# Optimization experiments

Hardware: AMD Instinct MI355X
Metric: run time of the kernel (lower is better)

## Reference

```python
import jax, jax.numpy as jnp
import numpy as np

IN_F = 4096
OUT_F = 4096
N = 16384


def setup_inputs() -> dict:
    key = jax.random.key(0)
    ks = jax.random.split(key, 7)
    return {
        "x": jax.random.normal(ks[0], (N, IN_F), dtype=jnp.float32),
        "weight_mu": jax.random.normal(ks[1], (OUT_F, IN_F), dtype=jnp.float32) * 0.1,
        "weight_rho": jax.random.normal(ks[2], (OUT_F, IN_F), dtype=jnp.float32) * 0.1,
        "bias_mu": jax.random.normal(ks[3], (OUT_F,), dtype=jnp.float32) * 0.1,
        "bias_rho": jax.random.normal(ks[4], (OUT_F,), dtype=jnp.float32) * 0.1,
        "eps_w": jax.random.normal(ks[5], (OUT_F, IN_F), dtype=jnp.float32),
        "eps_b": jax.random.normal(ks[6], (OUT_F,), dtype=jnp.float32),
    }


def reference(x, weight_mu, weight_rho, bias_mu, bias_rho, eps_w, eps_b):
    # softplus: log(1 + exp(rho)), written as log1p(exp(.)) for stability
    weight = weight_mu + jnp.log1p(jnp.exp(weight_rho)) * eps_w  # [out, in]
    bias = bias_mu + jnp.log1p(jnp.exp(bias_rho)) * eps_b        # [out]
    # F.linear(x, W, b) = x @ W.T + b
    return jnp.einsum("ni,oi->no", x, weight) + bias
```

## Files before the change

kernel.cpp:

```cpp
#include <hip/hip_runtime.h>
#include <hip/hip_bf16.h>

typedef unsigned short u16;
typedef __attribute__((ext_vector_type(4))) float f32x4;
typedef __attribute__((ext_vector_type(8))) short bf16x8;

__device__ __forceinline__ u16 f2bf(float f) {
    union { float f; unsigned u; } v; v.f = f;
    unsigned r = (v.u + 0x7fffu + ((v.u >> 16) & 1u)) >> 16;
    return (u16)r;
}

__device__ __forceinline__ float softplus(float x) {
    return (x > 15.f) ? x : log1pf(__expf(x));
}

__device__ __forceinline__ void gload_lds16(const void* g, void* l) {
    __builtin_amdgcn_global_load_lds(
        (__attribute__((address_space(1))) void*)(g),
        (__attribute__((address_space(3))) void*)(l),
        16, 0, 0);
}

#define BAR() do { asm volatile("" ::: "memory"); \
                   __builtin_amdgcn_s_barrier();  \
                   asm volatile("" ::: "memory"); } while (0)

#define DSR(dst, base, off) \
    asm volatile("ds_read_b128 %0, %1 offset:%2" : "=v"(dst) : "v"(base), "i"(off))

#define LGKM0_FENCE() do { \
    asm volatile("s_waitcnt lgkmcnt(0)" ::: "memory"); \
    __builtin_amdgcn_sched_barrier(0); } while (0)

__global__ __launch_bounds__(256) void prep_all(
        const float* __restrict__ x,
        const float* __restrict__ wmu, const float* __restrict__ wrho,
        const float* __restrict__ ew,
        const float* __restrict__ bmu, const float* __restrict__ brho,
        const float* __restrict__ eb,
        u16* __restrict__ xb, u16* __restrict__ wb, float* __restrict__ bs,
        int nx4, int nw4, int nb) {
    int i = blockIdx.x * 256 + threadIdx.x;
    if (i < nx4) {
        float4 v = ((const float4*)x)[i];
        ushort4 o;
        o.x = f2bf(v.x); o.y = f2bf(v.y); o.z = f2bf(v.z); o.w = f2bf(v.w);
        ((ushort4*)xb)[i] = o;
    }
    if (i < nw4) {
        float4 m = ((const float4*)wmu)[i];
        float4 r = ((const float4*)wrho)[i];
        float4 e = ((const float4*)ew)[i];
        ushort4 o;
        o.x = f2bf(m.x + softplus(r.x) * e.x);
        o.y = f2bf(m.y + softplus(r.y) * e.y);
        o.z = f2bf(m.z + softplus(r.z) * e.z);
        o.w = f2bf(m.w + softplus(r.w) * e.w);
        ((ushort4*)wb)[i] = o;
    }
    if (i < nb) {
        bs[i] = bmu[i] + softplus(brho[i]) * eb[i];
    }
}

template <int MB, int NB>
__device__ __forceinline__ void mfma_quad(f32x4 (&acc)[8][4],
                                          const bf16x8 (&av)[4][2],
                                          const bf16x8 (&bv)[2][2]) {
#pragma unroll
    for (int ks = 0; ks < 2; ++ks)
#pragma unroll
        for (int mi = 0; mi < 4; ++mi)
#pragma unroll
            for (int ni = 0; ni < 2; ++ni)
                acc[MB + mi][NB + ni] = __builtin_amdgcn_mfma_f32_16x16x32_bf16(
                    av[mi][ks], bv[ni][ks], acc[MB + mi][NB + ni], 0, 0, 0);
}

#define STAGE(region, h, P, koff) do {                                          \
    gload_lds16(P[h][0] + (koff), (char*)(region) + (h) * 16384 + (w * 2 + 0) * 1024); \
    gload_lds16(P[h][1] + (koff), (char*)(region) + (h) * 16384 + (w * 2 + 1) * 1024); \
} while (0)

#define RD_A(Rbyte, roff) do {                                         \
    unsigned r0a = aB0 + ((Rbyte) + (roff) * 128);                     \
    unsigned r1a = aB1 + ((Rbyte) + (roff) * 128);                     \
    DSR(a[0][0], r0a, 0);    DSR(a[0][1], r1a, 0);                     \
    DSR(a[1][0], r0a, 2048); DSR(a[1][1], r1a, 2048);                  \
    DSR(a[2][0], r0a, 4096); DSR(a[2][1], r1a, 4096);                  \
    DSR(a[3][0], r0a, 6144); DSR(a[3][1], r1a, 6144); } while (0)

#define RD_B(dst, Rbyte, roff) do {                                    \
    unsigned r0b = bB0 + ((Rbyte) + (roff) * 128);                     \
    unsigned r1b = bB1 + ((Rbyte) + (roff) * 128);                     \
    DSR(dst[0][0], r0b, 0);    DSR(dst[0][1], r1b, 0);                 \
    DSR(dst[1][0], r0b, 2048); DSR(dst[1][1], r1b, 2048); } while (0)

__global__ __launch_bounds__(512, 2) void gemm256_8ph(
        const u16* __restrict__ A,
        const u16* __restrict__ B,
        const float* __restrict__ bias,
        float* __restrict__ C,
        int M, int Nout, int K) {
    __shared__ __attribute__((aligned(16))) u16 smem[4][16384];

    const int tid  = threadIdx.x;
    const int lane = tid & 63;
    const int w    = tid >> 6;
    const int wr   = w >> 2;
    const int wc   = w & 3;

    u16* A0 = smem[0]; u16* B0 = smem[1];
    u16* A1 = smem[2]; u16* B1 = smem[3];

    const int nbn = Nout >> 8;
    const int nwg = (M >> 8) * nbn;
    const int cpx = nwg >> 3;
    const int swz = ((int)blockIdx.x & 7) * cpx + ((int)blockIdx.x >> 3);
    const int m0 = (swz / nbn) << 8;
    const int n0 = (swz % nbn) << 8;

    const u16* PA[2][2]; const u16* PB[2][2];
#pragma unroll
    for (int q = 0; q < 2; ++q) {
        int c   = (w * 2 + q) * 64 + lane;
        int row = c >> 3;
        int kc  = (c & 7) ^ (row & 7);
#pragma unroll
        for (int h = 0; h < 2; ++h) {
            PA[h][q] = A + (size_t)(m0 + h * 128 + row) * K + kc * 8;
            PB[h][q] = B + (size_t)(n0 + h * 128 + row) * K + kc * 8;
        }
    }

    const unsigned sb    = (unsigned)(size_t)(void*)&smem[0][0];
    const unsigned loff0 = (unsigned)((lane & 15) * 128 + (((lane >> 4) ^ (lane & 7)) & 7) * 16);
    const unsigned loff1 = (unsigned)((lane & 15) * 128 + ((((lane >> 4) + 4) ^ (lane & 7)) & 7) * 16);
    const unsigned aB0 = sb + (unsigned)(wr * 128 * 128) + loff0;
    const unsigned aB1 = sb + (unsigned)(wr * 128 * 128) + loff1;
    const unsigned bB0 = sb + (unsigned)(wc * 64 * 128) + loff0;
    const unsigned bB1 = sb + (unsigned)(wc * 64 * 128) + loff1;

    bf16x8 a[4][2], bl[2][2], bh[2][2];
    f32x4 acc[8][4] = {};

    const int NT = K >> 6;
    const int NI = NT >> 1;

    STAGE(B0, 0, PB, 0);  STAGE(B0, 1, PB, 0);
    STAGE(A0, 0, PA, 0);  STAGE(A0, 1, PA, 0);
    STAGE(B1, 0, PB, 64); STAGE(B1, 1, PB, 64);
    asm volatile("s_waitcnt vmcnt(4)" ::: "memory");
    BAR();
    RD_A(0, 0);

#pragma unroll 1
    for (int i = 0; i < NI; ++i) {
        int t2 = 2 * i + 2; if (t2 >= NT) t2 -= NT;
        int t3 = 2 * i + 3; if (t3 >= NT) t3 -= NT;
        const int k1 = (2 * i + 1) << 6;
        const int k2 = t2 << 6;
        const int k3 = t3 << 6;

        RD_B(bl, 32768, 0);
        STAGE(A1, 0, PA, k1);
        BAR();
        LGKM0_FENCE();
        __builtin_amdgcn_s_setprio(1);
        mfma_quad<0, 0>(acc, a, bl);
        __builtin_amdgcn_s_setprio(0);
        BAR();

        RD_B(bh, 32768, 32);
        STAGE(A1, 1, PA, k1);
        BAR();
        LGKM0_FENCE();
        __builtin_amdgcn_s_setprio(1);
        mfma_quad<0, 2>(acc, a, bh);
        __builtin_amdgcn_s_setprio(0);
        BAR();

        RD_A(0, 64);
        STAGE(B0, 0, PB, k2);
        BAR();
        LGKM0_FENCE();
        __builtin_amdgcn_s_setprio(1);
        mfma_quad<4, 2>(acc, a, bh);
        __builtin_amdgcn_s_setprio(0);
        BAR();

        STAGE(B0, 1, PB, k2);
        asm volatile("s_waitcnt vmcnt(4)" ::: "memory");
        BAR();
        __builtin_amdgcn_s_setprio(1);
        mfma_quad<4, 0>(acc, a, bl);
        __builtin_amdgcn_s_setprio(0);
        RD_A(65536, 0);
        BAR();

        RD_B(bl, 98304, 0);
        STAGE(A0, 0, PA, k2);
        BAR();
        LGKM0_FENCE();
        __builtin_amdgcn_s_setprio(1);
        mfma_quad<0, 0>(acc, a, bl);
        __builtin_amdgcn_s_setprio(0);
        BAR();

        RD_B(bh, 98304, 32);
        STAGE(A0, 1, PA, k2);
        BAR();
        LGKM0_FENCE();
        __builtin_amdgcn_s_setprio(1);
        mfma_quad<0, 2>(acc, a, bh);
        __builtin_amdgcn_s_setprio(0);
        BAR();

        RD_A(65536, 64);
        STAGE(B1, 0, PB, k3);
        BAR();
        LGKM0_FENCE();
        __builtin_amdgcn_s_setprio(1);
        mfma_quad<4, 2>(acc, a, bh);
        __builtin_amdgcn_s_setprio(0);
        BAR();

        STAGE(B1, 1, PB, k3);
        asm volatile("s_waitcnt vmcnt(4)" ::: "memory");
        BAR();
        __builtin_amdgcn_s_setprio(1);
        mfma_quad<4, 0>(acc, a, bl);
        __builtin_amdgcn_s_setprio(0);
        RD_A(0, 0);
        BAR();
    }

    asm volatile("s_waitcnt vmcnt(0) lgkmcnt(0)" ::: "memory");

    const int crow = (lane >> 4) * 4;
    const int ccol = lane & 15;
#pragma unroll
    for (int mi = 0; mi < 8; ++mi) {
#pragma unroll
        for (int ni = 0; ni < 4; ++ni) {
            const int row = m0 + wr * 128 + mi * 16 + crow;
            const int col = n0 + wc * 64 + ni * 16 + ccol;
            const float bv = bias[col];
            float* Cp = C + (size_t)row * Nout + col;
#pragma unroll
            for (int q = 0; q < 4; ++q)
                Cp[(size_t)q * Nout] = acc[mi][ni][q] + bv;
        }
    }
}

extern "C" void kernel_launch(void* const* d_in, const int* in_sizes, int n_in,
                              void* d_out, int out_size, void* d_ws, size_t ws_size,
                              hipStream_t stream) {
    const float* x    = (const float*)d_in[0];
    const float* wmu  = (const float*)d_in[1];
    const float* wrho = (const float*)d_in[2];
    const float* bmu  = (const float*)d_in[3];
    const float* brho = (const float*)d_in[4];
    const float* ew   = (const float*)d_in[5];
    const float* eb   = (const float*)d_in[6];
    float* out = (float*)d_out;

    const int Nout = in_sizes[3];
    const int K    = in_sizes[1] / Nout;
    const int M    = in_sizes[0] / K;

    u16* xb = (u16*)d_ws;
    u16* wb = xb + (size_t)M * K;
    float* bs = (float*)(wb + (size_t)Nout * K);

    const int nx4 = (M * K) / 4;
    const int nw4 = (Nout * K) / 4;
    prep_all<<<(nx4 + 255) / 256, 256, 0, stream>>>(
        x, wmu, wrho, ew, bmu, brho, eb, xb, wb, bs, nx4, nw4, Nout);

    dim3 grid((M / 256) * (Nout / 256));
    gemm256_8ph<<<grid, 512, 0, stream>>>(xb, wb, bs, out, M, Nout, K);
}
```

Measured before the change: 567.4 us.

## Switch GEMM to 128x128 tiles with full-fragment double-buffered register reads

Replaces the 256x256, 8-wave GEMM with a 128x128, 4-wave kernel. Each wave loads its full A/B fragments for a k-tile in one batch into double-buffered registers, cutting the number of LDS-read waits and barriers per phase. This trades less data reuse per block (more global/L2 traffic) for lower per-block register and LDS pressure and more blocks in flight.

```diff
diff --git a/kernel.cpp b/kernel.cpp
--- a/kernel.cpp
+++ b/kernel.cpp
@@ -29,7 +29,7 @@
 #define DSR(dst, base, off) \
     asm volatile("ds_read_b128 %0, %1 offset:%2" : "=v"(dst) : "v"(base), "i"(off))
 
-#define LGKM0_FENCE() do { \
+#define LGKM0() do { \
     asm volatile("s_waitcnt lgkmcnt(0)" ::: "memory"); \
     __builtin_amdgcn_sched_barrier(0); } while (0)
 
@@ -65,61 +65,61 @@
 }
 
 template <int MB, int NB>
-__device__ __forceinline__ void mfma_quad(f32x4 (&acc)[8][4],
-                                          const bf16x8 (&av)[4][2],
-                                          const bf16x8 (&bv)[2][2]) {
+__device__ __forceinline__ void quad8(f32x4 (&acc)[4][4],
+                                      const bf16x8 (&av)[4][2],
+                                      const bf16x8 (&bv)[4][2]) {
 #pragma unroll
     for (int ks = 0; ks < 2; ++ks)
 #pragma unroll
-        for (int mi = 0; mi < 4; ++mi)
+        for (int mi = 0; mi < 2; ++mi)
 #pragma unroll
             for (int ni = 0; ni < 2; ++ni)
                 acc[MB + mi][NB + ni] = __builtin_amdgcn_mfma_f32_16x16x32_bf16(
-                    av[mi][ks], bv[ni][ks], acc[MB + mi][NB + ni], 0, 0, 0);
-}
-
-#define STAGE(region, h, P, koff) do {                                          \
-    gload_lds16(P[h][0] + (koff), (char*)(region) + (h) * 16384 + (w * 2 + 0) * 1024); \
-    gload_lds16(P[h][1] + (koff), (char*)(region) + (h) * 16384 + (w * 2 + 1) * 1024); \
+                    av[MB + mi][ks], bv[NB + ni][ks], acc[MB + mi][NB + ni], 0, 0, 0);
+}
+
+#define STAGE(regionC, h, P, koff) do {                                         \
+    gload_lds16(P[h][0] + (koff), (regionC) + (h) * 8192 + (w * 2 + 0) * 1024); \
+    gload_lds16(P[h][1] + (koff), (regionC) + (h) * 8192 + (w * 2 + 1) * 1024); \
 } while (0)
 
-#define RD_A(Rbyte, roff) do {                                         \
-    unsigned r0a = aB0 + ((Rbyte) + (roff) * 128);                     \
-    unsigned r1a = aB1 + ((Rbyte) + (roff) * 128);                     \
-    DSR(a[0][0], r0a, 0);    DSR(a[0][1], r1a, 0);                     \
-    DSR(a[1][0], r0a, 2048); DSR(a[1][1], r1a, 2048);                  \
-    DSR(a[2][0], r0a, 4096); DSR(a[2][1], r1a, 4096);                  \
-    DSR(a[3][0], r0a, 6144); DSR(a[3][1], r1a, 6144); } while (0)
-
-#define RD_B(dst, Rbyte, roff) do {                                    \
-    unsigned r0b = bB0 + ((Rbyte) + (roff) * 128);                     \
-    unsigned r1b = bB1 + ((Rbyte) + (roff) * 128);                     \
-    DSR(dst[0][0], r0b, 0);    DSR(dst[0][1], r1b, 0);                 \
-    DSR(dst[1][0], r0b, 2048); DSR(dst[1][1], r1b, 2048); } while (0)
-
-__global__ __launch_bounds__(512, 2) void gemm256_8ph(
+#define RD_TILE(af, bf, R) do {                                        \
+    unsigned _a0 = aB0 + (R), _a1 = aB1 + (R);                         \
+    unsigned _b0 = bB0 + (R), _b1 = bB1 + (R);                         \
+    DSR(bf[0][0], _b0, 0);    DSR(bf[1][0], _b0, 2048);                \
+    DSR(bf[0][1], _b1, 0);    DSR(bf[1][1], _b1, 2048);                \
+    DSR(af[0][0], _a0, 0);    DSR(af[1][0], _a0, 2048);                \
+    DSR(af[0][1], _a1, 0);    DSR(af[1][1], _a1, 2048);                \
+    DSR(bf[2][0], _b0, 4096); DSR(bf[3][0], _b0, 6144);                \
+    DSR(bf[2][1], _b1, 4096); DSR(bf[3][1], _b1, 6144);                \
+    DSR(af[2][0], _a0, 4096); DSR(af[3][0], _a0, 6144);                \
+    DSR(af[2][1], _a1, 4096); DSR(af[3][1], _a1, 6144); } while (0)
+
+__global__ __launch_bounds__(256, 2) void gemm128_fr(
         const u16* __restrict__ A,
         const u16* __restrict__ B,
         const float* __restrict__ bias,
         float* __restrict__ C,
         int M, int Nout, int K) {
-    __shared__ __attribute__((aligned(16))) u16 smem[4][16384];
+    __shared__ __attribute__((aligned(16))) u16 smem[4][8192];
 
     const int tid  = threadIdx.x;
     const int lane = tid & 63;
     const int w    = tid >> 6;
-    const int wr   = w >> 2;
-    const int wc   = w & 3;
-
-    u16* A0 = smem[0]; u16* B0 = smem[1];
-    u16* A1 = smem[2]; u16* B1 = smem[3];
-
-    const int nbn = Nout >> 8;
-    const int nwg = (M >> 8) * nbn;
+    const int wr   = w >> 1;
+    const int wc   = w & 1;
+
+    char* RA0 = (char*)smem;
+    char* RB0 = (char*)smem + 16384;
+    char* RA1 = (char*)smem + 32768;
+    char* RB1 = (char*)smem + 49152;
+
+    const int nbn = Nout >> 7;
+    const int nwg = (M >> 7) * nbn;
     const int cpx = nwg >> 3;
     const int swz = ((int)blockIdx.x & 7) * cpx + ((int)blockIdx.x >> 3);
-    const int m0 = (swz / nbn) << 8;
-    const int n0 = (swz % nbn) << 8;
+    const int m0 = (swz / nbn) << 7;
+    const int n0 = (swz % nbn) << 7;
 
     const u16* PA[2][2]; const u16* PB[2][2];
 #pragma unroll
@@ -129,31 +129,31 @@
         int kc  = (c & 7) ^ (row & 7);
 #pragma unroll
         for (int h = 0; h < 2; ++h) {
-            PA[h][q] = A + (size_t)(m0 + h * 128 + row) * K + kc * 8;
-            PB[h][q] = B + (size_t)(n0 + h * 128 + row) * K + kc * 8;
+            PA[h][q] = A + (size_t)(m0 + h * 64 + row) * K + kc * 8;
+            PB[h][q] = B + (size_t)(n0 + h * 64 + row) * K + kc * 8;
         }
     }
 
     const unsigned sb    = (unsigned)(size_t)(void*)&smem[0][0];
     const unsigned loff0 = (unsigned)((lane & 15) * 128 + (((lane >> 4) ^ (lane & 7)) & 7) * 16);
     const unsigned loff1 = (unsigned)((lane & 15) * 128 + ((((lane >> 4) + 4) ^ (lane & 7)) & 7) * 16);
-    const unsigned aB0 = sb + (unsigned)(wr * 128 * 128) + loff0;
-    const unsigned aB1 = sb + (unsigned)(wr * 128 * 128) + loff1;
-    const unsigned bB0 = sb + (unsigned)(wc * 64 * 128) + loff0;
-    const unsigned bB1 = sb + (unsigned)(wc * 64 * 128) + loff1;
-
-    bf16x8 a[4][2], bl[2][2], bh[2][2];
-    f32x4 acc[8][4] = {};
+    const unsigned aB0 = sb + (unsigned)(wr * 64 * 128) + loff0;
+    const unsigned aB1 = sb + (unsigned)(wr * 64 * 128) + loff1;
+    const unsigned bB0 = sb + 16384u + (unsigned)(wc * 64 * 128) + loff0;
+    const unsigned bB1 = sb + 16384u + (unsigned)(wc * 64 * 128) + loff1;
+
+    bf16x8 a0f[4][2], b0f[4][2], a1f[4][2], b1f[4][2];
+    f32x4 acc[4][4] = {};
 
     const int NT = K >> 6;
     const int NI = NT >> 1;
 
-    STAGE(B0, 0, PB, 0);  STAGE(B0, 1, PB, 0);
-    STAGE(A0, 0, PA, 0);  STAGE(A0, 1, PA, 0);
-    STAGE(B1, 0, PB, 64); STAGE(B1, 1, PB, 64);
+    STAGE(RB0, 0, PB, 0);  STAGE(RB0, 1, PB, 0);
+    STAGE(RA0, 0, PA, 0);  STAGE(RA0, 1, PA, 0);
+    STAGE(RB1, 0, PB, 64); STAGE(RB1, 1, PB, 64);
     asm volatile("s_waitcnt vmcnt(4)" ::: "memory");
     BAR();
-    RD_A(0, 0);
+    RD_TILE(a0f, b0f, 0);
 
 #pragma unroll 1
     for (int i = 0; i < NI; ++i) {
@@ -163,77 +163,61 @@
         const int k2 = t2 << 6;
         const int k3 = t3 << 6;
 
-        RD_B(bl, 32768, 0);
-        STAGE(A1, 0, PA, k1);
-        BAR();
-        LGKM0_FENCE();
-        __builtin_amdgcn_s_setprio(1);
-        mfma_quad<0, 0>(acc, a, bl);
-        __builtin_amdgcn_s_setprio(0);
-        BAR();
-
-        RD_B(bh, 32768, 32);
-        STAGE(A1, 1, PA, k1);
-        BAR();
-        LGKM0_FENCE();
-        __builtin_amdgcn_s_setprio(1);
-        mfma_quad<0, 2>(acc, a, bh);
-        __builtin_amdgcn_s_setprio(0);
-        BAR();
-
-        RD_A(0, 64);
-        STAGE(B0, 0, PB, k2);
-        BAR();
-        LGKM0_FENCE();
-        __builtin_amdgcn_s_setprio(1);
-        mfma_quad<4, 2>(acc, a, bh);
-        __builtin_amdgcn_s_setprio(0);
-        BAR();
-
-        STAGE(B0, 1, PB, k2);
+        STAGE(RA1, 0, PA, k1);
+        BAR();
+        LGKM0();
+        __builtin_amdgcn_s_setprio(1);
+        quad8<0, 0>(acc, a0f, b0f);
+        __builtin_amdgcn_s_setprio(0);
+
+        STAGE(RA1, 1, PA, k1);
+        BAR();
+        __builtin_amdgcn_s_setprio(1);
+        quad8<0, 2>(acc, a0f, b0f);
+        __builtin_amdgcn_s_setprio(0);
+
+        STAGE(RB0, 0, PB, k2);
+        BAR();
+        __builtin_amdgcn_s_setprio(1);
+        quad8<2, 2>(acc, a0f, b0f);
+        __builtin_amdgcn_s_setprio(0);
+
+        STAGE(RB0, 1, PB, k2);
         asm volatile("s_waitcnt vmcnt(4)" ::: "memory");
         BAR();
-        __builtin_amdgcn_s_setprio(1);
-        mfma_quad<4, 0>(acc, a, bl);
-        __builtin_amdgcn_s_setprio(0);
-        RD_A(65536, 0);
-        BAR();
-
-        RD_B(bl, 98304, 0);
-        STAGE(A0, 0, PA, k2);
-        BAR();
-        LGKM0_FENCE();
-        __builtin_amdgcn_s_setprio(1);
-        mfma_quad<0, 0>(acc, a, bl);
-        __builtin_amdgcn_s_setprio(0);
-        BAR();
-
-        RD_B(bh, 98304, 32);
-        STAGE(A0, 1, PA, k2);
-        BAR();
-        LGKM0_FENCE();
-        __builtin_amdgcn_s_setprio(1);
-        mfma_quad<0, 2>(acc, a, bh);
-        __builtin_amdgcn_s_setprio(0);
-        BAR();
-
-        RD_A(65536, 64);
-        STAGE(B1, 0, PB, k3);
-        BAR();
-        LGKM0_FENCE();
-        __builtin_amdgcn_s_setprio(1);
-        mfma_quad<4, 2>(acc, a, bh);
-        __builtin_amdgcn_s_setprio(0);
-        BAR();
-
-        STAGE(B1, 1, PB, k3);
+        RD_TILE(a1f, b1f, 32768);
+        __builtin_amdgcn_sched_barrier(0);
+        __builtin_amdgcn_s_setprio(1);
+        quad8<2, 0>(acc, a0f, b0f);
+        __builtin_amdgcn_s_setprio(0);
+
+        STAGE(RA0, 0, PA, k2);
+        BAR();
+        LGKM0();
+        __builtin_amdgcn_s_setprio(1);
+        quad8<0, 0>(acc, a1f, b1f);
+        __builtin_amdgcn_s_setprio(0);
+
+        STAGE(RA0, 1, PA, k2);
+        BAR();
+        __builtin_amdgcn_s_setprio(1);
+        quad8<0, 2>(acc, a1f, b1f);
+        __builtin_amdgcn_s_setprio(0);
+
+        STAGE(RB1, 0, PB, k3);
+        BAR();
+        __builtin_amdgcn_s_setprio(1);
+        quad8<2, 2>(acc, a1f, b1f);
+        __builtin_amdgcn_s_setprio(0);
+
+        STAGE(RB1, 1, PB, k3);
         asm volatile("s_waitcnt vmcnt(4)" ::: "memory");
         BAR();
-        __builtin_amdgcn_s_setprio(1);
-        mfma_quad<4, 0>(acc, a, bl);
-        __builtin_amdgcn_s_setprio(0);
-        RD_A(0, 0);
-        BAR();
+        RD_TILE(a0f, b0f, 0);
+        __builtin_amdgcn_sched_barrier(0);
+        __builtin_amdgcn_s_setprio(1);
+        quad8<2, 0>(acc, a1f, b1f);
+        __builtin_amdgcn_s_setprio(0);
     }
 
     asm volatile("s_waitcnt vmcnt(0) lgkmcnt(0)" ::: "memory");
@@ -241,10 +225,10 @@
     const int crow = (lane >> 4) * 4;
     const int ccol = lane & 15;
 #pragma unroll
-    for (int mi = 0; mi < 8; ++mi) {
+    for (int mi = 0; mi < 4; ++mi) {
 #pragma unroll
         for (int ni = 0; ni < 4; ++ni) {
-            const int row = m0 + wr * 128 + mi * 16 + crow;
+            const int row = m0 + wr * 64 + mi * 16 + crow;
             const int col = n0 + wc * 64 + ni * 16 + ccol;
             const float bv = bias[col];
             float* Cp = C + (size_t)row * Nout + col;
@@ -280,6 +264,6 @@
     prep_all<<<(nx4 + 255) / 256, 256, 0, stream>>>(
         x, wmu, wrho, ew, bmu, brho, eb, xb, wb, bs, nx4, nw4, Nout);
 
-    dim3 grid((M / 256) * (Nout / 256));
-    gemm256_8ph<<<grid, 512, 0, stream>>>(xb, wb, bs, out, M, Nout, K);
-}
+    dim3 grid((M / 128) * (Nout / 128));
+    gemm128_fr<<<grid, 256, 0, stream>>>(xb, wb, bs, out, M, Nout, K);
+}
```

Measured after the change: 816.2 us. +43.8%, slower.
